# Optimization experiments

Measured on AMD Instinct MI355X. Metric: run time of the kernel, lower is better.

Reference implementation:

```python
import jax, jax.numpy as jnp
import numpy as np

DIM = 128
HEADS = 4
DH = 32
SCALE = DH ** -0.5


def _ln(x, g, b):
    m = x.mean(-1, keepdims=True)
    v = x.var(-1, keepdims=True)
    return (x - m) / jnp.sqrt(v + 1e-5) * g + b


def setup_inputs() -> dict:
    key = jax.random.key(0)
    ks = jax.random.split(key, 16)
    B, N, H, W, HK, WK = 2, 6, 48, 48, 24, 24
    d, hd = DIM, HEADS * DH
    p = lambda k, s: (jax.random.normal(k, s, jnp.float32) * 0.02)
    return {
        "q": jax.random.normal(ks[0], (B, N, d, H, W), jnp.float32),
        "k": jax.random.normal(ks[1], (B, N, d, HK, WK), jnp.float32),
        "v": jax.random.normal(ks[2], (B, N, d, HK, WK), jnp.float32),
        "skip": jax.random.normal(ks[3], (B, d, H, W), jnp.float32),
        "lnq_g": jnp.ones(d), "lnq_b": jnp.zeros(d),
        "Wq": p(ks[4], (d, hd)), "bq": jnp.zeros(hd),
        "lnk_g": jnp.ones(d), "lnk_b": jnp.zeros(d),
        "Wk": p(ks[5], (d, hd)), "bk": jnp.zeros(hd),
        "lnv_g": jnp.ones(d), "lnv_b": jnp.zeros(d),
        "Wv": p(ks[6], (d, hd)), "bv": jnp.zeros(hd),
        "Wp": p(ks[7], (hd, d)), "bp": jnp.zeros(d),
        "pre_g": jnp.ones(d), "pre_b": jnp.zeros(d),
        "W1": p(ks[8], (d, 2 * d)), "b1": jnp.zeros(2 * d),
        "W2": p(ks[9], (2 * d, d)), "b2": jnp.zeros(d),
        "post_g": jnp.ones(d), "post_b": jnp.zeros(d),
    }


def reference(q, k, v, skip, lnq_g, lnq_b, Wq, bq, lnk_g, lnk_b, Wk, bk,
              lnv_g, lnv_b, Wv, bv, Wp, bp, pre_g, pre_b, W1, b1, W2, b2,
              post_g, post_b):
    B, N, d, H, W = q.shape
    _, _, _, HK, WK = k.shape
    Q, K = H * W, HK * WK
    # b n d H W -> b n (H W) d
    qx = q.transpose(0, 1, 3, 4, 2).reshape(B, N, Q, d)
    kx = k.transpose(0, 1, 3, 4, 2).reshape(B, N, K, d)
    vx = v.transpose(0, 1, 3, 4, 2).reshape(B, N * K, d)
    # norm + linear projections
    qp = _ln(qx, lnq_g, lnq_b) @ Wq + bq  # (B,N,Q,HEADS*DH)
    kp = _ln(kx, lnk_g, lnk_b) @ Wk + bk
    vp = _ln(vx, lnv_g, lnv_b) @ Wv + bv  # (B,N*K,HEADS*DH)
    # split heads: b ... (m d) -> (b m) ... d
    qp = qp.reshape(B, N, Q, HEADS, DH).transpose(0, 3, 1, 2, 4).reshape(B * HEADS, N, Q, DH)
    kp = kp.reshape(B, N, K, HEADS, DH).transpose(0, 3, 1, 2, 4).reshape(B * HEADS, N, K, DH)
    vp = vp.reshape(B, N * K, HEADS, DH).transpose(0, 2, 1, 3).reshape(B * HEADS, N * K, DH)
    # per-view scores, then softmax jointly over (n K)
    scores = SCALE * jnp.einsum('bnqd,bnkd->bnqk', qp, kp)
    scores = scores.transpose(0, 2, 1, 3).reshape(B * HEADS, Q, N * K)
    a = jax.nn.softmax(scores, axis=-1)
    out = jnp.einsum('bqk,bkd->bqd', a, vp)  # (B*HEADS, Q, DH)
    # merge heads: (b m) Q d -> b Q (m d)
    z = out.reshape(B, HEADS, Q, DH).transpose(0, 2, 1, 3).reshape(B, Q, HEADS * DH)
    z = z @ Wp + bp
    z = z + skip.transpose(0, 2, 3, 1).reshape(B, Q, d)
    z = _ln(z, pre_g, pre_b)
    z = z + (jax.nn.gelu(z @ W1 + b1, approximate=False) @ W2 + b2)
    z = _ln(z, post_g, post_b)
    return z.reshape(B, H, W, d).transpose(0, 3, 1, 2)
```

## Files before the change

### kernel.cpp

```cpp
#include <hip/hip_runtime.h>
#include <cmath>

#define B_    2
#define N_    6
#define D_    128
#define Q_    2304
#define K_    576
#define NK_   3456
#define HEADS_ 4
#define DH_   32
#define SCALE_ 0.17677669529663687f

typedef __attribute__((ext_vector_type(8))) short bf16x8;
typedef __attribute__((ext_vector_type(4))) float f32x4;

#if defined(__has_builtin)
#if __has_builtin(__builtin_amdgcn_cvt_pk_bf16_f32)
#define HAS_PK_BF16 1
#endif
#endif

static __device__ __forceinline__ unsigned short f2bf(float f) {
  union { float f; unsigned u; } x; x.f = f;
  unsigned u = x.u + 0x7fffu + ((x.u >> 16) & 1u);
  return (unsigned short)(u >> 16);
}
static __device__ __forceinline__ unsigned pkbf(float a, float b) {
#ifdef HAS_PK_BF16
  typedef __attribute__((ext_vector_type(2))) __bf16 vbf2;
  union { vbf2 v; unsigned u; } cv;
  cv.v = __builtin_amdgcn_cvt_pk_bf16_f32(a, b);
  return cv.u;
#else
  return (unsigned)f2bf(a) | ((unsigned)f2bf(b) << 16);
#endif
}

__global__ __launch_bounds__(256) void k_prep_wt(
    const float* __restrict__ Wq, const float* __restrict__ Wk,
    const float* __restrict__ Wv, const float* __restrict__ Wp,
    const float* __restrict__ W1, const float* __restrict__ W2,
    unsigned short* __restrict__ WTq, unsigned short* __restrict__ WTk,
    unsigned short* __restrict__ WTv, unsigned short* __restrict__ WTp,
    unsigned short* __restrict__ WT1, unsigned short* __restrict__ WT2)
{
  __shared__ float tile[32][33];
  const int wb = blockIdx.x, t = threadIdx.x;
  const float* src; unsigned short* dst; int Kd, J, tl;
  if      (wb < 16) { src = Wq; dst = WTq; Kd = 128; J = 128; tl = wb; }
  else if (wb < 32) { src = Wk; dst = WTk; Kd = 128; J = 128; tl = wb - 16; }
  else if (wb < 48) { src = Wv; dst = WTv; Kd = 128; J = 128; tl = wb - 32; }
  else if (wb < 64) { src = Wp; dst = WTp; Kd = 128; J = 128; tl = wb - 48; }
  else if (wb < 96) { src = W1; dst = WT1; Kd = 128; J = 256; tl = wb - 64; }
  else              { src = W2; dst = WT2; Kd = 256; J = 128; tl = wb - 96; }
  const int njt = J >> 5;
  const int tj = tl % njt, tk = tl / njt;
#pragma unroll
  for (int i = 0; i < 4; ++i) {
    int idx = t + 256 * i;
    int r = idx >> 5, c = idx & 31;
    tile[r][c] = src[(size_t)(tk * 32 + r) * J + tj * 32 + c];
  }
  __syncthreads();
#pragma unroll
  for (int i = 0; i < 2; ++i) {
    int idx = t + 256 * i;
    int rr = idx >> 4, c2 = (idx & 15) << 1;
    *(unsigned*)&dst[(size_t)(tj * 32 + rr) * Kd + tk * 32 + c2] =
        pkbf(tile[c2][rr], tile[c2 + 1][rr]);
  }
}

__global__ __launch_bounds__(256) void k_ln_proj_all(
    const float* __restrict__ qin, const float* __restrict__ kin,
    const float* __restrict__ vin,
    const float* __restrict__ lnq_g, const float* __restrict__ lnq_b,
    const float* __restrict__ lnk_g, const float* __restrict__ lnk_b,
    const float* __restrict__ lnv_g, const float* __restrict__ lnv_b,
    const unsigned short* __restrict__ WTq, const unsigned short* __restrict__ WTk,
    const unsigned short* __restrict__ WTv,
    const float* __restrict__ bq, const float* __restrict__ bk,
    const float* __restrict__ bv,
    unsigned short* __restrict__ QPh, unsigned short* __restrict__ KPh,
    unsigned short* __restrict__ VPTh)
{
  __shared__ float xs[32][132];
  __shared__ unsigned short xh[32][136];
  __shared__ float gs[128], bs[128];
  __shared__ float mu[32], rsd[32];
  const int t = threadIdx.x;
  const int bid = blockIdx.x;

  const float* x; const unsigned short* WT; const float* g; const float* bl;
  const float* bias; int S, blk, mode; float osc;
  if (bid < 864)       { mode = 0; blk = bid;        x = qin; WT = WTq; g = lnq_g; bl = lnq_b; bias = bq; S = Q_; osc = SCALE_; }
  else if (bid < 1080) { mode = 0; blk = bid - 864;  x = kin; WT = WTk; g = lnk_g; bl = lnk_b; bias = bk; S = K_; osc = 1.0f; }
  else                 { mode = 1; blk = bid - 1080; x = vin; WT = WTv; g = lnv_g; bl = lnv_b; bias = bv; S = K_; osc = 1.0f; }
  const int ntile = S >> 5;
  const int o  = blk / ntile;
  const int s0 = (blk % ntile) << 5;

  if (t < 128) { gs[t] = g[t]; bs[t] = bl[t]; }
  const float* xb = x + (size_t)o * 128 * (size_t)S + s0;
#pragma unroll
  for (int i = 0; i < 4; ++i) {
    int idx = t + 256 * i;
    int c = idx >> 3, s4 = (idx & 7) << 2;
    float4 xv = *(const float4*)&xb[(size_t)c * S + s4];
    xs[s4 + 0][c] = xv.x; xs[s4 + 1][c] = xv.y;
    xs[s4 + 2][c] = xv.z; xs[s4 + 3][c] = xv.w;
  }
  __syncthreads();
  {
    int s = t >> 3, l8 = t & 7;
    float sum = 0.f, sq = 0.f;
    for (int c = l8; c < 128; c += 8) { float v = xs[s][c]; sum += v; sq += v * v; }
#pragma unroll
    for (int off = 4; off > 0; off >>= 1) {
      sum += __shfl_down(sum, off, 8);
      sq  += __shfl_down(sq,  off, 8);
    }
    if (l8 == 0) {
      float mth = sum * 0.0078125f;
      float var = sq * 0.0078125f - mth * mth;
      mu[s] = mth; rsd[s] = rsqrtf(var + 1e-5f);
    }
  }
  __syncthreads();
#pragma unroll
  for (int i = 0; i < 8; ++i) {
    int idx = t + 256 * i;
    int s = idx >> 6, c2 = (idx & 63) << 1;
    float y0 = (xs[s][c2]     - mu[s]) * rsd[s] * gs[c2]     + bs[c2];
    float y1 = (xs[s][c2 + 1] - mu[s]) * rsd[s] * gs[c2 + 1] + bs[c2 + 1];
    *(unsigned*)&xh[s][c2] = pkbf(y0, y1);
  }
  __syncthreads();
  const int w = t >> 6, lane = t & 63, quad = lane >> 4, l16 = lane & 15;
  const f32x4 zf = {0.f, 0.f, 0.f, 0.f};
  f32x4 acc[2][2] = {{zf, zf}, {zf, zf}};
#pragma unroll
  for (int kc = 0; kc < 4; ++kc) {
    bf16x8 a0 = *(const bf16x8*)&xh[l16][kc * 32 + quad * 8];
    bf16x8 a1 = *(const bf16x8*)&xh[16 + l16][kc * 32 + quad * 8];
    bf16x8 b0 = *(const bf16x8*)&WT[(size_t)(w * 32 + l16) * 128 + kc * 32 + quad * 8];
    bf16x8 b1 = *(const bf16x8*)&WT[(size_t)(w * 32 + 16 + l16) * 128 + kc * 32 + quad * 8];
    acc[0][0] = __builtin_amdgcn_mfma_f32_16x16x32_bf16(a0, b0, acc[0][0], 0, 0, 0);
    acc[0][1] = __builtin_amdgcn_mfma_f32_16x16x32_bf16(a0, b1, acc[0][1], 0, 0, 0);
    acc[1][0] = __builtin_amdgcn_mfma_f32_16x16x32_bf16(a1, b0, acc[1][0], 0, 0, 0);
    acc[1][1] = __builtin_amdgcn_mfma_f32_16x16x32_bf16(a1, b1, acc[1][1], 0, 0, 0);
  }
  if (mode == 0) {
    unsigned short* outh = (bid < 864) ? QPh : KPh;
    __syncthreads();
#pragma unroll
    for (int mt = 0; mt < 2; ++mt)
#pragma unroll
      for (int nt = 0; nt < 2; ++nt) {
        int col = w * 32 + nt * 16 + l16;
        float bc = bias[col];
#pragma unroll
        for (int r = 0; r < 4; ++r)
          xh[mt * 16 + quad * 4 + r][col] = f2bf((acc[mt][nt][r] + bc) * osc);
      }
    __syncthreads();
#pragma unroll
    for (int i = 0; i < 2; ++i) {
      int s = i * 16 + (t >> 4), c8 = (t & 15) << 3;
      *(uint4*)&outh[((size_t)o * S + s0 + s) * 128 + c8] = *(uint4*)&xh[s][c8];
    }
  } else {
    const int b = o / 6, n = o % 6;
#pragma unroll
    for (int mt = 0; mt < 2; ++mt)
#pragma unroll
      for (int nt = 0; nt < 2; ++nt) {
        int col = w * 32 + nt * 16 + l16;
        int hh = col >> 5, dh = col & 31;
        float bc = bias[col];
        ushort4 pk;
        *(unsigned*)&pk.x = pkbf(acc[mt][nt][0] + bc, acc[mt][nt][1] + bc);
        *(unsigned*)&pk.z = pkbf(acc[mt][nt][2] + bc, acc[mt][nt][3] + bc);
        int s = n * 576 + s0 + mt * 16 + quad * 4;
        *(ushort4*)&VPTh[((size_t)(b * 4 + hh) * 32 + dh) * (size_t)NK_ + s] = pk;
      }
  }
}

__global__ __launch_bounds__(256) void k_attn_mfma(
    const unsigned short* __restrict__ QPh, const unsigned short* __restrict__ KPh,
    const unsigned short* __restrict__ VPTh, float* __restrict__ PO,
    float* __restrict__ Pl)
{
  __shared__ __align__(16) char smem_u[10240];
  unsigned short (*plds)[2][16][40] = (unsigned short (*)[2][16][40])smem_u;
  float (*ol)[16][32] = (float (*)[16][32])smem_u;
  __shared__ float ll[4][2][4][16];
  const int t = threadIdx.x;
  const int w = t >> 6, lane = t & 63;
  const int quad = lane >> 4, l16 = lane & 15;
  const int qt = blockIdx.x % 72;
  const int rest = blockIdx.x / 72;
  const int bhx = rest >> 1, ks = rest & 1;
  const int bb = bhx >> 2, h = bhx & 3;
  const int q0 = qt << 5;

  const unsigned short* vbase = VPTh + (size_t)bhx * 32 * (size_t)NK_;
  const f32x4 zf = {0.f, 0.f, 0.f, 0.f};
  f32x4 o00 = zf, o01 = zf, o10 = zf, o11 = zf;
  float lsum0 = 0.f, lsum1 = 0.f;

  const int m8 = ks * 4 + w;
  int c0 = (108 * m8) >> 3, c1 = (108 * (m8 + 1)) >> 3;

  while (c0 < c1) {
    const int nn = c0 / 18;
    const int cend = min(c1, (nn + 1) * 18);
    const unsigned short* kb = &KPh[((size_t)(bb * 6 + nn) * K_) * 128 + h * 32];
    const unsigned short* qb = &QPh[((size_t)(bb * 6 + nn) * Q_ + q0) * 128 + h * 32];
    bf16x8 qc0 = *(const bf16x8*)&qb[(size_t)l16 * 128 + quad * 8];
    bf16x8 qc1 = *(const bf16x8*)&qb[(size_t)(16 + l16) * 128 + quad * 8];

    int kl = (c0 - nn * 18) << 5;
    bf16x8 kf0 = *(const bf16x8*)&kb[(size_t)(kl + l16) * 128 + quad * 8];
    bf16x8 kf1 = *(const bf16x8*)&kb[(size_t)(kl + 16 + l16) * 128 + quad * 8];
    const unsigned short* vb = vbase + ((size_t)c0 << 5);
    bf16x8 vf0 = *(const bf16x8*)&vb[(size_t)l16 * NK_ + quad * 8];
    bf16x8 vf1 = *(const bf16x8*)&vb[(size_t)(16 + l16) * NK_ + quad * 8];

    for (int kc = c0; kc < cend; ++kc) {
      const int kln = (kc + 1 - nn * 18) << 5;
      bf16x8 nk0 = *(const bf16x8*)&kb[(size_t)(kln + l16) * 128 + quad * 8];
      bf16x8 nk1 = *(const bf16x8*)&kb[(size_t)(kln + 16 + l16) * 128 + quad * 8];
      const unsigned short* vbn = vbase + ((size_t)(kc + 1) << 5);
      bf16x8 nv0 = *(const bf16x8*)&vbn[(size_t)l16 * NK_ + quad * 8];
      bf16x8 nv1 = *(const bf16x8*)&vbn[(size_t)(16 + l16) * NK_ + quad * 8];

      f32x4 s00 = __builtin_amdgcn_mfma_f32_16x16x32_bf16(kf0, qc0, zf, 0, 0, 0);
      f32x4 s01 = __builtin_amdgcn_mfma_f32_16x16x32_bf16(kf1, qc0, zf, 0, 0, 0);
      f32x4 s10 = __builtin_amdgcn_mfma_f32_16x16x32_bf16(kf0, qc1, zf, 0, 0, 0);
      f32x4 s11 = __builtin_amdgcn_mfma_f32_16x16x32_bf16(kf1, qc1, zf, 0, 0, 0);

      float a00 = __expf(fminf(s00.x, 70.f)), a01 = __expf(fminf(s00.y, 70.f));
      float a02 = __expf(fminf(s00.z, 70.f)), a03 = __expf(fminf(s00.w, 70.f));
      float a10 = __expf(fminf(s01.x, 70.f)), a11 = __expf(fminf(s01.y, 70.f));
      float a12 = __expf(fminf(s01.z, 70.f)), a13 = __expf(fminf(s01.w, 70.f));
      lsum0 += (a00 + a01 + a02 + a03) + (a10 + a11 + a12 + a13);
      float b00 = __expf(fminf(s10.x, 70.f)), b01 = __expf(fminf(s10.y, 70.f));
      float b02 = __expf(fminf(s10.z, 70.f)), b03 = __expf(fminf(s10.w, 70.f));
      float b10 = __expf(fminf(s11.x, 70.f)), b11 = __expf(fminf(s11.y, 70.f));
      float b12 = __expf(fminf(s11.z, 70.f)), b13 = __expf(fminf(s11.w, 70.f));
      lsum1 += (b00 + b01 + b02 + b03) + (b10 + b11 + b12 + b13);

      uint2 w0a; w0a.x = pkbf(a00, a01); w0a.y = pkbf(a02, a03);
      uint2 w0b; w0b.x = pkbf(a10, a11); w0b.y = pkbf(a12, a13);
      uint2 w1a; w1a.x = pkbf(b00, b01); w1a.y = pkbf(b02, b03);
      uint2 w1b; w1b.x = pkbf(b10, b11); w1b.y = pkbf(b12, b13);
      *(uint2*)&plds[w][0][l16][quad * 4]      = w0a;
      *(uint2*)&plds[w][0][l16][16 + quad * 4] = w0b;
      *(uint2*)&plds[w][1][l16][quad * 4]      = w1a;
      *(uint2*)&plds[w][1][l16][16 + quad * 4] = w1b;
      bf16x8 pf0 = *(const bf16x8*)&plds[w][0][l16][quad * 8];
      bf16x8 pf1 = *(const bf16x8*)&plds[w][1][l16][quad * 8];

      o00 = __builtin_amdgcn_mfma_f32_16x16x32_bf16(pf0, vf0, o00, 0, 0, 0);
      o01 = __builtin_amdgcn_mfma_f32_16x16x32_bf16(pf0, vf1, o01, 0, 0, 0);
      o10 = __builtin_amdgcn_mfma_f32_16x16x32_bf16(pf1, vf0, o10, 0, 0, 0);
      o11 = __builtin_amdgcn_mfma_f32_16x16x32_bf16(pf1, vf1, o11, 0, 0, 0);

      kf0 = nk0; kf1 = nk1; vf0 = nv0; vf1 = nv1;
    }
    c0 = cend;
  }

  ll[w][0][quad][l16] = lsum0;
  ll[w][1][quad][l16] = lsum1;
#pragma unroll
  for (int tt = 0; tt < 2; ++tt) {
    __syncthreads();
    f32x4 t0 = tt ? o10 : o00;
    f32x4 t1 = tt ? o11 : o01;
#pragma unroll
    for (int r = 0; r < 4; ++r) {
      ol[w][quad * 4 + r][l16]      = t0[r];
      ol[w][quad * 4 + r][16 + l16] = t1[r];
    }
    __syncthreads();
    const int q = t >> 4, i16 = t & 15, dd = i16 << 1;
    float a0 = 0.f, a1 = 0.f;
#pragma unroll
    for (int ww = 0; ww < 4; ++ww) { a0 += ol[ww][q][dd]; a1 += ol[ww][q][dd + 1]; }
    float2 r2; r2.x = a0; r2.y = a1;
    *(float2*)&PO[(((size_t)ks * 8 + bhx) * Q_ + q0 + tt * 16 + q) * 32 + dd] = r2;
    if (i16 == 0) {
      float l = 0.f;
#pragma unroll
      for (int ww = 0; ww < 4; ++ww)
#pragma unroll
        for (int qq = 0; qq < 4; ++qq) l += ll[ww][tt][qq][q];
      Pl[((size_t)ks * 8 + bhx) * Q_ + q0 + tt * 16 + q] = l;
    }
  }
}

__global__ __launch_bounds__(512) void k_tail(
    const float* __restrict__ PO, const float* __restrict__ Pl,
    const unsigned short* __restrict__ WTp, const float* __restrict__ bp,
    const float* __restrict__ skip,
    const float* __restrict__ pre_g, const float* __restrict__ pre_b,
    const unsigned short* __restrict__ WT1, const float* __restrict__ b1,
    const unsigned short* __restrict__ WT2, const float* __restrict__ b2,
    const float* __restrict__ post_g, const float* __restrict__ post_b,
    float* __restrict__ out)
{
  __shared__ float xs[16][132];
  __shared__ unsigned short xh[16][136];
  __shared__ unsigned short hb[16][264];
  __shared__ float g1s[128], b1s[128], g2s[128], b2s[128];
  __shared__ float mu[16], rsd[16];
  const int t = threadIdx.x;
  const int row0 = blockIdx.x << 4;
  const int bb = row0 / Q_, hw0 = row0 % Q_;
  const int w = t >> 6, lane = t & 63, quad = lane >> 4, l16 = lane & 15;
  const f32x4 zf = {0.f, 0.f, 0.f, 0.f};

  if (t < 128) { g1s[t] = pre_g[t]; b1s[t] = pre_b[t]; g2s[t] = post_g[t]; b2s[t] = post_b[t]; }
#pragma unroll
  for (int i = 0; i < 2; ++i) {
    int idx = t + 512 * i;
    int s = idx >> 6, c2 = (idx & 63) << 1;
    int q = hw0 + s;
    int h = c2 >> 5, dh = c2 & 31;
    size_t bq = (size_t)(bb * 4 + h) * Q_ + q;
    size_t i0 = bq * 32 + dh;
    float2 p0 = *(const float2*)&PO[i0];
    float2 p1 = *(const float2*)&PO[589824 + i0];
    float inv = 1.f / (Pl[bq] + Pl[18432 + bq]);
    *(unsigned*)&xh[s][c2] = pkbf((p0.x + p1.x) * inv, (p0.y + p1.y) * inv);
  }
  __syncthreads();
  {
    f32x4 acc = zf;
    const int col = w * 16 + l16;
#pragma unroll
    for (int kc = 0; kc < 4; ++kc) {
      bf16x8 a0 = *(const bf16x8*)&xh[l16][kc * 32 + quad * 8];
      bf16x8 b0 = *(const bf16x8*)&WTp[(size_t)col * 128 + kc * 32 + quad * 8];
      acc = __builtin_amdgcn_mfma_f32_16x16x32_bf16(a0, b0, acc, 0, 0, 0);
    }
    float bc = bp[col];
    float4 sk = *(const float4*)&skip[((size_t)bb * 128 + col) * Q_ + hw0 + quad * 4];
    xs[quad * 4 + 0][col] = acc[0] + bc + sk.x;
    xs[quad * 4 + 1][col] = acc[1] + bc + sk.y;
    xs[quad * 4 + 2][col] = acc[2] + bc + sk.z;
    xs[quad * 4 + 3][col] = acc[3] + bc + sk.w;
  }
  __syncthreads();
  {
    int s = t >> 5, lg = t & 31;
    float sum = 0.f, sq = 0.f;
    for (int c = lg; c < 128; c += 32) { float v = xs[s][c]; sum += v; sq += v * v; }
#pragma unroll
    for (int off = 16; off > 0; off >>= 1) {
      sum += __shfl_down(sum, off, 32);
      sq  += __shfl_down(sq,  off, 32);
    }
    if (lg == 0) {
      float mth = sum * 0.0078125f;
      float var = sq * 0.0078125f - mth * mth;
      mu[s] = mth; rsd[s] = rsqrtf(var + 1e-5f);
    }
  }
  __syncthreads();
#pragma unroll
  for (int i = 0; i < 2; ++i) {
    int idx = t + 512 * i;
    int s = idx >> 6, c2 = (idx & 63) << 1;
    float y0 = (xs[s][c2]     - mu[s]) * rsd[s] * g1s[c2]     + b1s[c2];
    float y1 = (xs[s][c2 + 1] - mu[s]) * rsd[s] * g1s[c2 + 1] + b1s[c2 + 1];
    xs[s][c2] = y0; xs[s][c2 + 1] = y1;
    *(unsigned*)&xh[s][c2] = pkbf(y0, y1);
  }
  __syncthreads();
  {
#pragma unroll
    for (int nt = 0; nt < 2; ++nt) {
      const int col = w * 32 + nt * 16 + l16;
      f32x4 acc = zf;
#pragma unroll
      for (int kc = 0; kc < 4; ++kc) {
        bf16x8 a0 = *(const bf16x8*)&xh[l16][kc * 32 + quad * 8];
        bf16x8 b0 = *(const bf16x8*)&WT1[(size_t)col * 128 + kc * 32 + quad * 8];
        acc = __builtin_amdgcn_mfma_f32_16x16x32_bf16(a0, b0, acc, 0, 0, 0);
      }
      float bc = b1[col];
#pragma unroll
      for (int r = 0; r < 4; ++r) {
        float hx = acc[r] + bc;
        hb[quad * 4 + r][col] =
            f2bf(0.5f * hx * (1.f + erff(hx * 0.7071067811865476f)));
      }
    }
  }
  __syncthreads();
  {
    f32x4 acc = zf;
    const int col = w * 16 + l16;
#pragma unroll
    for (int kc = 0; kc < 8; ++kc) {
      bf16x8 a0 = *(const bf16x8*)&hb[l16][kc * 32 + quad * 8];
      bf16x8 b0 = *(const bf16x8*)&WT2[(size_t)col * 256 + kc * 32 + quad * 8];
      acc = __builtin_amdgcn_mfma_f32_16x16x32_bf16(a0, b0, acc, 0, 0, 0);
    }
    float bc = b2[col];
#pragma unroll
    for (int r = 0; r < 4; ++r) {
      int row = quad * 4 + r;
      xs[row][col] = acc[r] + bc + xs[row][col];
    }
  }
  __syncthreads();
  {
    int s = t >> 5, lg = t & 31;
    float sum = 0.f, sq = 0.f;
    for (int c = lg; c < 128; c += 32) { float v = xs[s][c]; sum += v; sq += v * v; }
#pragma unroll
    for (int off = 16; off > 0; off >>= 1) {
      sum += __shfl_down(sum, off, 32);
      sq  += __shfl_down(sq,  off, 32);
    }
    if (lg == 0) {
      float mth = sum * 0.0078125f;
      float var = sq * 0.0078125f - mth * mth;
      mu[s] = mth; rsd[s] = rsqrtf(var + 1e-5f);
    }
  }
  __syncthreads();
#pragma unroll
  for (int i = 0; i < 4; ++i) {
    int idx = t + 512 * i;
    int s = idx & 15, c = idx >> 4;
    out[(size_t)bb * (128 * (size_t)Q_) + (size_t)c * Q_ + hw0 + s] =
        (xs[s][c] - mu[s]) * rsd[s] * g2s[c] + b2s[c];
  }
}

extern "C" void kernel_launch(void* const* d_in, const int* in_sizes, int n_in,
                              void* d_out, int out_size, void* d_ws, size_t ws_size,
                              hipStream_t stream) {
  const float* q     = (const float*)d_in[0];
  const float* k     = (const float*)d_in[1];
  const float* v     = (const float*)d_in[2];
  const float* skip  = (const float*)d_in[3];
  const float* lnq_g = (const float*)d_in[4];
  const float* lnq_b = (const float*)d_in[5];
  const float* Wq    = (const float*)d_in[6];
  const float* bq    = (const float*)d_in[7];
  const float* lnk_g = (const float*)d_in[8];
  const float* lnk_b = (const float*)d_in[9];
  const float* Wk    = (const float*)d_in[10];
  const float* bk    = (const float*)d_in[11];
  const float* lnv_g = (const float*)d_in[12];
  const float* lnv_b = (const float*)d_in[13];
  const float* Wv    = (const float*)d_in[14];
  const float* bvv   = (const float*)d_in[15];
  const float* Wp    = (const float*)d_in[16];
  const float* bp    = (const float*)d_in[17];
  const float* pre_g = (const float*)d_in[18];
  const float* pre_b = (const float*)d_in[19];
  const float* W1    = (const float*)d_in[20];
  const float* b1    = (const float*)d_in[21];
  const float* W2    = (const float*)d_in[22];
  const float* b2    = (const float*)d_in[23];
  const float* post_g= (const float*)d_in[24];
  const float* post_b= (const float*)d_in[25];
  float* out = (float*)d_out;

  unsigned short* QPh  = (unsigned short*)d_ws;
  unsigned short* KPh  = QPh + 3538944;
  unsigned short* VPTh = KPh + 884736;
  float* PO  = (float*)(VPTh + 884736);
  float* Pl  = PO + 1179648;
  unsigned short* WTq = (unsigned short*)(Pl + 36864);
  unsigned short* WTk = WTq + 16384;
  unsigned short* WTv = WTk + 16384;
  unsigned short* WTp = WTv + 16384;
  unsigned short* WT1 = WTp + 16384;
  unsigned short* WT2 = WT1 + 32768;

  k_prep_wt<<<dim3(128), dim3(256), 0, stream>>>(Wq, Wk, Wv, Wp, W1, W2,
                                                 WTq, WTk, WTv, WTp, WT1, WT2);
  k_ln_proj_all<<<dim3(1296), dim3(256), 0, stream>>>(
      q, k, v, lnq_g, lnq_b, lnk_g, lnk_b, lnv_g, lnv_b,
      WTq, WTk, WTv, bq, bk, bvv, QPh, KPh, VPTh);
  k_attn_mfma<<<dim3(1152), dim3(256), 0, stream>>>(QPh, KPh, VPTh, PO, Pl);
  k_tail<<<dim3(288), dim3(512), 0, stream>>>(PO, Pl, WTp, bp, skip,
                                              pre_g, pre_b, WT1, b1, WT2, b2,
                                              post_g, post_b, out);
}
```

Baseline: 176.9 us.

## Software-pipeline QK^T MFMAs ahead of softmax and fold log2e into Q scale

Restructures the attention inner loop so the score MFMAs for the next key chunk are issued right after the PV MFMAs of the current chunk, overlapping matrix work with the exp/pack/LDS phase. The P tile in LDS is double-buffered so consecutive iterations do not overwrite data still being read. The Q projection scale now includes log2(e), so exp2f replaces __expf and the clamp at 70 is dropped. In exchange the kernel uses more registers and twice the LDS, and overflow protection is removed.

After: 175.3 us. About the same (-0.9%).

```diff
diff --git a/kernel.cpp b/kernel.cpp
--- a/kernel.cpp
+++ b/kernel.cpp
@@ -10,6 +10,7 @@
 #define HEADS_ 4
 #define DH_   32
 #define SCALE_ 0.17677669529663687f
+#define SCLOG2E_ 0.25504672615621814f
 
 typedef __attribute__((ext_vector_type(8))) short bf16x8;
 typedef __attribute__((ext_vector_type(4))) float f32x4;
@@ -93,7 +94,7 @@
 
   const float* x; const unsigned short* WT; const float* g; const float* bl;
   const float* bias; int S, blk, mode; float osc;
-  if (bid < 864)       { mode = 0; blk = bid;        x = qin; WT = WTq; g = lnq_g; bl = lnq_b; bias = bq; S = Q_; osc = SCALE_; }
+  if (bid < 864)       { mode = 0; blk = bid;        x = qin; WT = WTq; g = lnq_g; bl = lnq_b; bias = bq; S = Q_; osc = SCLOG2E_; }
   else if (bid < 1080) { mode = 0; blk = bid - 864;  x = kin; WT = WTk; g = lnk_g; bl = lnk_b; bias = bk; S = K_; osc = 1.0f; }
   else                 { mode = 1; blk = bid - 1080; x = vin; WT = WTv; g = lnv_g; bl = lnv_b; bias = bv; S = K_; osc = 1.0f; }
   const int ntile = S >> 5;
@@ -192,8 +193,9 @@
     const unsigned short* __restrict__ VPTh, float* __restrict__ PO,
     float* __restrict__ Pl)
 {
-  __shared__ __align__(16) char smem_u[10240];
-  unsigned short (*plds)[2][16][40] = (unsigned short (*)[2][16][40])smem_u;
+  __shared__ __align__(16) char smem_u[20480];
+  typedef unsigned short plds_t[2][2][16][40];
+  plds_t* plds = (plds_t*)smem_u;
   float (*ol)[16][32] = (float (*)[16][32])smem_u;
   __shared__ float ll[4][2][4][16];
   const int t = threadIdx.x;
@@ -209,6 +211,7 @@
   const f32x4 zf = {0.f, 0.f, 0.f, 0.f};
   f32x4 o00 = zf, o01 = zf, o10 = zf, o11 = zf;
   float lsum0 = 0.f, lsum1 = 0.f;
+  int buf = 0;
 
   const int m8 = ks * 4 + w;
   int c0 = (108 * m8) >> 3, c1 = (108 * (m8 + 1)) >> 3;
@@ -225,8 +228,12 @@
     bf16x8 kf0 = *(const bf16x8*)&kb[(size_t)(kl + l16) * 128 + quad * 8];
     bf16x8 kf1 = *(const bf16x8*)&kb[(size_t)(kl + 16 + l16) * 128 + quad * 8];
     const unsigned short* vb = vbase + ((size_t)c0 << 5);
-    bf16x8 vf0 = *(const bf16x8*)&vb[(size_t)l16 * NK_ + quad * 8];
-    bf16x8 vf1 = *(const bf16x8*)&vb[(size_t)(16 + l16) * NK_ + quad * 8];
+    bf16x8 pv0 = *(const bf16x8*)&vb[(size_t)l16 * NK_ + quad * 8];
+    bf16x8 pv1 = *(const bf16x8*)&vb[(size_t)(16 + l16) * NK_ + quad * 8];
+    f32x4 s00 = __builtin_amdgcn_mfma_f32_16x16x32_bf16(kf0, qc0, zf, 0, 0, 0);
+    f32x4 s01 = __builtin_amdgcn_mfma_f32_16x16x32_bf16(kf1, qc0, zf, 0, 0, 0);
+    f32x4 s10 = __builtin_amdgcn_mfma_f32_16x16x32_bf16(kf0, qc1, zf, 0, 0, 0);
+    f32x4 s11 = __builtin_amdgcn_mfma_f32_16x16x32_bf16(kf1, qc1, zf, 0, 0, 0);
 
     for (int kc = c0; kc < cend; ++kc) {
       const int kln = (kc + 1 - nn * 18) << 5;
@@ -236,39 +243,39 @@
       bf16x8 nv0 = *(const bf16x8*)&vbn[(size_t)l16 * NK_ + quad * 8];
       bf16x8 nv1 = *(const bf16x8*)&vbn[(size_t)(16 + l16) * NK_ + quad * 8];
 
-      f32x4 s00 = __builtin_amdgcn_mfma_f32_16x16x32_bf16(kf0, qc0, zf, 0, 0, 0);
-      f32x4 s01 = __builtin_amdgcn_mfma_f32_16x16x32_bf16(kf1, qc0, zf, 0, 0, 0);
-      f32x4 s10 = __builtin_amdgcn_mfma_f32_16x16x32_bf16(kf0, qc1, zf, 0, 0, 0);
-      f32x4 s11 = __builtin_amdgcn_mfma_f32_16x16x32_bf16(kf1, qc1, zf, 0, 0, 0);
-
-      float a00 = __expf(fminf(s00.x, 70.f)), a01 = __expf(fminf(s00.y, 70.f));
-      float a02 = __expf(fminf(s00.z, 70.f)), a03 = __expf(fminf(s00.w, 70.f));
-      float a10 = __expf(fminf(s01.x, 70.f)), a11 = __expf(fminf(s01.y, 70.f));
-      float a12 = __expf(fminf(s01.z, 70.f)), a13 = __expf(fminf(s01.w, 70.f));
+      float a00 = exp2f(s00.x), a01 = exp2f(s00.y);
+      float a02 = exp2f(s00.z), a03 = exp2f(s00.w);
+      float a10 = exp2f(s01.x), a11 = exp2f(s01.y);
+      float a12 = exp2f(s01.z), a13 = exp2f(s01.w);
       lsum0 += (a00 + a01 + a02 + a03) + (a10 + a11 + a12 + a13);
-      float b00 = __expf(fminf(s10.x, 70.f)), b01 = __expf(fminf(s10.y, 70.f));
-      float b02 = __expf(fminf(s10.z, 70.f)), b03 = __expf(fminf(s10.w, 70.f));
-      float b10 = __expf(fminf(s11.x, 70.f)), b11 = __expf(fminf(s11.y, 70.f));
-      float b12 = __expf(fminf(s11.z, 70.f)), b13 = __expf(fminf(s11.w, 70.f));
+      float b00 = exp2f(s10.x), b01 = exp2f(s10.y);
+      float b02 = exp2f(s10.z), b03 = exp2f(s10.w);
+      float b10 = exp2f(s11.x), b11 = exp2f(s11.y);
+      float b12 = exp2f(s11.z), b13 = exp2f(s11.w);
       lsum1 += (b00 + b01 + b02 + b03) + (b10 + b11 + b12 + b13);
 
       uint2 w0a; w0a.x = pkbf(a00, a01); w0a.y = pkbf(a02, a03);
       uint2 w0b; w0b.x = pkbf(a10, a11); w0b.y = pkbf(a12, a13);
       uint2 w1a; w1a.x = pkbf(b00, b01); w1a.y = pkbf(b02, b03);
       uint2 w1b; w1b.x = pkbf(b10, b11); w1b.y = pkbf(b12, b13);
-      *(uint2*)&plds[w][0][l16][quad * 4]      = w0a;
-      *(uint2*)&plds[w][0][l16][16 + quad * 4] = w0b;
-      *(uint2*)&plds[w][1][l16][quad * 4]      = w1a;
-      *(uint2*)&plds[w][1][l16][16 + quad * 4] = w1b;
-      bf16x8 pf0 = *(const bf16x8*)&plds[w][0][l16][quad * 8];
-      bf16x8 pf1 = *(const bf16x8*)&plds[w][1][l16][quad * 8];
-
-      o00 = __builtin_amdgcn_mfma_f32_16x16x32_bf16(pf0, vf0, o00, 0, 0, 0);
-      o01 = __builtin_amdgcn_mfma_f32_16x16x32_bf16(pf0, vf1, o01, 0, 0, 0);
-      o10 = __builtin_amdgcn_mfma_f32_16x16x32_bf16(pf1, vf0, o10, 0, 0, 0);
-      o11 = __builtin_amdgcn_mfma_f32_16x16x32_bf16(pf1, vf1, o11, 0, 0, 0);
-
-      kf0 = nk0; kf1 = nk1; vf0 = nv0; vf1 = nv1;
+      *(uint2*)&plds[w][buf][0][l16][quad * 4]      = w0a;
+      *(uint2*)&plds[w][buf][0][l16][16 + quad * 4] = w0b;
+      *(uint2*)&plds[w][buf][1][l16][quad * 4]      = w1a;
+      *(uint2*)&plds[w][buf][1][l16][16 + quad * 4] = w1b;
+      bf16x8 pf0 = *(const bf16x8*)&plds[w][buf][0][l16][quad * 8];
+      bf16x8 pf1 = *(const bf16x8*)&plds[w][buf][1][l16][quad * 8];
+
+      o00 = __builtin_amdgcn_mfma_f32_16x16x32_bf16(pf0, pv0, o00, 0, 0, 0);
+      o01 = __builtin_amdgcn_mfma_f32_16x16x32_bf16(pf0, pv1, o01, 0, 0, 0);
+      o10 = __builtin_amdgcn_mfma_f32_16x16x32_bf16(pf1, pv0, o10, 0, 0, 0);
+      o11 = __builtin_amdgcn_mfma_f32_16x16x32_bf16(pf1, pv1, o11, 0, 0, 0);
+
+      s00 = __builtin_amdgcn_mfma_f32_16x16x32_bf16(nk0, qc0, zf, 0, 0, 0);
+      s01 = __builtin_amdgcn_mfma_f32_16x16x32_bf16(nk1, qc0, zf, 0, 0, 0);
+      s10 = __builtin_amdgcn_mfma_f32_16x16x32_bf16(nk0, qc1, zf, 0, 0, 0);
+      s11 = __builtin_amdgcn_mfma_f32_16x16x32_bf16(nk1, qc1, zf, 0, 0, 0);
+      pv0 = nv0; pv1 = nv1;
+      buf ^= 1;
     }
     c0 = cend;
   }
```
